# Optimization experiments

Hardware: AMD Instinct MI355X
Metric: run time of the kernel (lower is better)

Reference implementation:

```python
import jax, jax.numpy as jnp
import numpy as np

NUM_GROUPS = 32
EPS = 1e-5


def group_norm(x, gamma, beta):
    # x: [B, C, H, W]; normalize per group of C//NUM_GROUPS channels over (c_in_group, H, W)
    B, C, H, W = x.shape
    xg = x.reshape(B, NUM_GROUPS, C // NUM_GROUPS, H, W)
    mean = jnp.mean(xg, axis=(2, 3, 4), keepdims=True)
    var = jnp.var(xg, axis=(2, 3, 4), keepdims=True)
    xn = ((xg - mean) * jax.lax.rsqrt(var + EPS)).reshape(B, C, H, W)
    return xn * gamma[None, :, None, None] + beta[None, :, None, None]


def setup_inputs() -> dict:
    key = jax.random.key(0)
    kx, kq, kp = jax.random.split(key, 3)
    B, C, H, W = 4, 256, 64, 64
    x = jax.random.normal(kx, (B, C, H, W), dtype=jnp.float32)
    gamma = jnp.ones((C,), dtype=jnp.float32)
    beta = jnp.zeros((C,), dtype=jnp.float32)
    # 1x1 convs == channel matmuls; weights [out_c, in_c]
    w_qkv = jax.random.normal(kq, (3 * C, C), dtype=jnp.float32) / np.sqrt(C)
    w_proj = jax.random.normal(kp, (C, C), dtype=jnp.float32) / np.sqrt(C)
    return {"x": x, "t": 0, "gamma": gamma, "beta": beta, "w_qkv": w_qkv, "w_proj": w_proj}


def reference(x, t, gamma, beta, w_qkv, w_proj):
    B, C, H, W = x.shape
    normed = group_norm(x, gamma, beta)  # [B,C,H,W]
    qkv = jnp.einsum('bchw,oc->bohw', normed, w_qkv)  # [B,3C,H,W]
    q, k, v = jnp.split(qkv, 3, axis=1)
    N = H * W
    q = q.reshape(B, C, N)
    k = k.reshape(B, C, N)
    v = v.reshape(B, C, N)
    # scores[b,i,j] = sum_c q[b,c,i] k[b,c,j] / sqrt(C)
    scores = jnp.einsum('bci,bcj->bij', q, k) / jnp.sqrt(jnp.asarray(C, x.dtype))
    attn = jax.nn.softmax(scores, axis=-1)  # [B,N,N]
    # out[b,c,i] = sum_j v[b,c,j] attn[b,i,j]
    out = jnp.einsum('bcj,bij->bci', v, attn).reshape(B, C, H, W)
    out = jnp.einsum('bchw,oc->bohw', out, w_proj)
    return x + out
```

## Files before the change

### kernel.cpp

```cpp
#include <hip/hip_runtime.h>

typedef __bf16 bf16x8 __attribute__((ext_vector_type(8)));
typedef float floatx4 __attribute__((ext_vector_type(4)));
typedef float floatx16 __attribute__((ext_vector_type(16)));
typedef unsigned int u32;
typedef unsigned long long u64;

#define BB 4
#define CC 256
#define NN 4096

__device__ __forceinline__ unsigned short f2bf(float f) {
  union { float f; unsigned u; } v; v.f = f;
  unsigned r = v.u + 0x7fffu + ((v.u >> 16) & 1u);
  return (unsigned short)(r >> 16);
}

__device__ __forceinline__ float bf2f(unsigned short s) {
  union { unsigned u; float f; } v; v.u = ((u32)s) << 16;
  return v.f;
}

__device__ __forceinline__ void async16(const void* g, void* l) {
  __builtin_amdgcn_global_load_lds((const __attribute__((address_space(1))) u32*)g,
                                   (__attribute__((address_space(3))) u32*)l, 16, 0, 0);
}

__device__ __forceinline__ u32 fbits(float f) {
  union { float f; u32 u; } v; v.f = f; return v.u;
}

__global__ __launch_bounds__(256) void gn_fused(const float* __restrict__ x,
                                                const float* __restrict__ gamma, const float* __restrict__ beta,
                                                unsigned short* __restrict__ normed,
                                                const float* __restrict__ wqkv, const float* __restrict__ wproj,
                                                unsigned short* __restrict__ wq_bf, unsigned short* __restrict__ wp_bf) {
  int t = threadIdx.x;
  if (blockIdx.x >= 128) {
    int base = (blockIdx.x - 128) * 1024;
#pragma unroll
    for (int j = 0; j < 4; ++j) {
      int i = base + j * 256 + t;
      if (i < 196608) {
        float v = wqkv[i];
        if (i < 65536) v *= 0.090168440055560213f;
        wq_bf[i] = f2bf(v);
      } else {
        wp_bf[i - 196608] = f2bf(wproj[i - 196608]);
      }
    }
    return;
  }

  __shared__ __attribute__((aligned(16))) char smem[65928];
  unsigned short* xs = (unsigned short*)smem;
  float* par = (float*)(smem + 65664);

  int bg = blockIdx.x;
  int g = bg & 31;
  const float* p = x + (size_t)bg * 32768;
  float s = 0.f, q = 0.f;
#pragma unroll
  for (int it = 0; it < 32; ++it) {
    int idx = it * 1024 + t * 4;
    float4 v = *(const float4*)(p + idx);
    s += v.x + v.y + v.z + v.w;
    q += v.x * v.x + v.y * v.y + v.z * v.z + v.w * v.w;
    u64 pk = (u64)f2bf(v.x) | ((u64)f2bf(v.y) << 16) | ((u64)f2bf(v.z) << 32) | ((u64)f2bf(v.w) << 48);
    int row = idx >> 12, col = idx & 4095;
    *(u64*)&xs[row * 4104 + col] = pk;
  }
#pragma unroll
  for (int off = 1; off < 64; off <<= 1) {
    s += __shfl_xor(s, off, 64);
    q += __shfl_xor(q, off, 64);
  }
  int w = t >> 6;
  if ((t & 63) == 0) { par[32 + w] = s; par[40 + w] = q; }
  __syncthreads();
  if (t == 0) {
    float S = par[32] + par[33] + par[34] + par[35];
    float Q = par[40] + par[41] + par[42] + par[43];
    float mean = S * (1.f / 32768.f);
    float var = Q * (1.f / 32768.f) - mean * mean;
    par[16] = mean;
    par[17] = rsqrtf(var + 1e-5f);
  }
  __syncthreads();
  if (t < 8) {
    float mean = par[16], rstd = par[17];
    float sc = rstd * gamma[g * 8 + t];
    par[t] = sc;
    par[8 + t] = beta[g * 8 + t] - mean * sc;
  }
  __syncthreads();
  float scv[8], shv[8];
#pragma unroll
  for (int c = 0; c < 8; ++c) { scv[c] = par[c]; shv[c] = par[8 + c]; }
  unsigned short* ob = normed + (size_t)bg * 4096 * 8;
#pragma unroll
  for (int k = 0; k < 16; ++k) {
    int n = k * 256 + t;
    union { unsigned short us[8]; uint4 qv; } o;
#pragma unroll
    for (int c = 0; c < 8; ++c) {
      float xv = bf2f(xs[c * 4104 + n]);
      o.us[c] = f2bf(xv * scv[c] + shv[c]);
    }
    *(uint4*)(ob + (size_t)n * 8) = o.qv;
  }
}

__global__ __launch_bounds__(256, 2) void gemm_qkv_v(const unsigned short* __restrict__ normed,
                                                     const unsigned short* __restrict__ wq_bf,
                                                     const unsigned short* __restrict__ wv_bf,
                                                     unsigned short* __restrict__ qkbuf,
                                                     unsigned short* __restrict__ vbuf) {
  __shared__ __attribute__((aligned(16))) char smem[65536];
  int b = blockIdx.y;
  const unsigned short *Ab, *Bb;
  unsigned short* Cb;
  int ldc, m0, n0;
  bool aBlocked;
  if (blockIdx.x < 128) {
    int mt = blockIdx.x % 32, nt = blockIdx.x / 32;
    m0 = mt * 128; n0 = nt * 128;
    Ab = normed + (size_t)b * NN * 8 * 32;
    Bb = wq_bf + (size_t)n0 * 256;
    Cb = qkbuf + (size_t)b * NN * 512;
    ldc = 512;
    aBlocked = true;
  } else {
    int xx = blockIdx.x - 128;
    int mt = xx & 1, nt = xx >> 1;
    m0 = mt * 128; n0 = nt * 128;
    Ab = wv_bf + (size_t)m0 * 256;
    Bb = normed + (size_t)b * NN * 8 * 32;
    Cb = vbuf + (size_t)b * CC * NN;
    ldc = NN;
    aBlocked = false;
  }
  int t = threadIdx.x, w = t >> 6, l = t & 63;
  int l16 = l & 15, quad = l >> 4;
  int wr = w >> 1, wc = w & 1;

  auto stage = [&](int kb, int buf) {
    int rsub = l >> 3;
    int cj = (l & 7) ^ rsub;
    char* ab = smem + buf * 16384;
    char* bb = smem + 32768 + buf * 16384;
#pragma unroll
    for (int it = 0; it < 4; ++it) {
      int pp = w * 4 + it;
      int row = 8 * pp + rsub;
      size_t goLin = (size_t)row * 256 + kb * 64 + cj * 8;
      if (aBlocked) {
        size_t goA = ((size_t)(kb * 8 + cj) * 4096 + m0 + row) * 8;
        async16(Ab + goA, ab + pp * 1024);
        async16(Bb + goLin, bb + pp * 1024);
      } else {
        size_t goB = ((size_t)(kb * 8 + cj) * 4096 + n0 + row) * 8;
        async16(Ab + goLin, ab + pp * 1024);
        async16(Bb + goB, bb + pp * 1024);
      }
    }
  };

  floatx4 acc[4][4];
#pragma unroll
  for (int m = 0; m < 4; ++m)
#pragma unroll
    for (int n = 0; n < 4; ++n)
#pragma unroll
      for (int r = 0; r < 4; ++r) acc[m][n][r] = 0.f;

  stage(0, 0);

#pragma unroll 1
  for (int kb = 0; kb < 4; ++kb) {
    int cur = kb & 1;
    __syncthreads();
    if (kb < 3) stage(kb + 1, cur ^ 1);
    const unsigned short* As = (const unsigned short*)(smem + cur * 16384);
    const unsigned short* Bs = (const unsigned short*)(smem + 32768 + cur * 16384);
#pragma unroll
    for (int kk = 0; kk < 2; ++kk) {
      bf16x8 af[4], bfr[4];
      int sw = ((kk * 4 + quad) ^ (l16 & 7)) * 8;
#pragma unroll
      for (int m = 0; m < 4; ++m)
        af[m] = *(const bf16x8*)&As[(wr * 64 + m * 16 + l16) * 64 + sw];
#pragma unroll
      for (int n = 0; n < 4; ++n)
        bfr[n] = *(const bf16x8*)&Bs[(wc * 64 + n * 16 + l16) * 64 + sw];
#pragma unroll
      for (int m = 0; m < 4; ++m)
#pragma unroll
        for (int n = 0; n < 4; ++n)
          acc[m][n] = __builtin_amdgcn_mfma_f32_16x16x32_bf16(af[m], bfr[n], acc[m][n], 0, 0, 0);
    }
  }

#pragma unroll
  for (int m = 0; m < 4; ++m)
#pragma unroll
    for (int n = 0; n < 4; ++n)
#pragma unroll
      for (int r = 0; r < 4; ++r) {
        int row = m0 + wr * 64 + m * 16 + quad * 4 + r;
        int col = n0 + wc * 64 + n * 16 + l16;
        Cb[(size_t)row * ldc + col] = f2bf(acc[m][n][r]);
      }
}

__global__ __launch_bounds__(512, 2) void attn(const unsigned short* __restrict__ qk,
                                               const unsigned short* __restrict__ vbuf,
                                               unsigned short* __restrict__ opart0,
                                               unsigned short* __restrict__ opart1,
                                               float* __restrict__ lpart) {
  __shared__ __attribute__((aligned(16))) char smem[131072];

  int xcd = blockIdx.x & 7, slot = blockIdx.x >> 3;
  int b = xcd >> 1;
  int kh = xcd & 1;
  int i0 = slot * 128;
  int k0 = kh * 32;

  int t = threadIdx.x, w = t >> 6, l = t & 63;
  int l31 = l & 31, hi = l >> 5;
  int jh = w & 1;
  int iq = w >> 1;

  const size_t bqk = (size_t)b * NN * 512;
  const size_t bv = (size_t)b * CC * NN;

  auto stage = [&](int tile, int buf) {
    const unsigned short* kg = qk + bqk + (size_t)tile * 64 * 512 + 256;
    char* kb = smem + buf * 32768;
#pragma unroll
    for (int it = 0; it < 4; ++it) {
      int pp = w * 4 + it;
      int r = 2 * pp + (l >> 5);
      int c = (l & 31) ^ (r & 31);
      async16(kg + (size_t)r * 512 + c * 8, kb + pp * 1024);
    }
    const unsigned short* vg = vbuf + bv + (size_t)tile * 64;
    char* vb = smem + 65536 + buf * 32768;
    int cj = (l & 7) ^ ((l >> 3) & 7);
#pragma unroll
    for (int it = 0; it < 4; ++it) {
      int pp = w * 4 + it;
      int rc = 8 * pp + (l >> 3);
      async16(vg + (size_t)rc * NN + cj * 8, vb + pp * 1024);
    }
  };

  stage(k0, 0);

  bf16x8 qreg[16];
  {
    const unsigned short* qp = qk + bqk + (size_t)(i0 + iq * 32 + l31) * 512 + hi * 8;
#pragma unroll
    for (int ks = 0; ks < 16; ++ks)
      qreg[ks] = *(const bf16x8*)(qp + ks * 16);
  }

  floatx16 oacc[8];
#pragma unroll
  for (int cf = 0; cf < 8; ++cf)
#pragma unroll
    for (int r = 0; r < 16; ++r) oacc[cf][r] = 0.f;
  float lacc = 0.f;

  for (int kt = 0; kt < 32; ++kt) {
    int cur = kt & 1;
    __syncthreads();
    if (kt < 31) stage(k0 + kt + 1, cur ^ 1);

    const unsigned short* Kc = (const unsigned short*)(smem + cur * 32768);
    const unsigned short* Vc = (const unsigned short*)(smem + 65536 + cur * 32768);

    floatx16 st;
#pragma unroll
    for (int r = 0; r < 16; ++r) st[r] = 0.f;
#pragma unroll
    for (int ks = 0; ks < 16; ++ks) {
      bf16x8 kf = *(const bf16x8*)&Kc[(jh * 32 + l31) * 256 + (((ks << 1) | hi) ^ l31) * 8];
      st = __builtin_amdgcn_mfma_f32_32x32x16_bf16(kf, qreg[ks], st, 0, 0, 0);
    }

    u32 pr[8];
#pragma unroll
    for (int k2 = 0; k2 < 8; ++k2) {
      float p0 = __builtin_amdgcn_exp2f(st[2 * k2]);
      float p1 = __builtin_amdgcn_exp2f(st[2 * k2 + 1]);
      lacc += p0 + p1;
      pr[k2] = __builtin_amdgcn_perm(fbits(p1), fbits(p0), 0x07060302u);
    }

    union U { u32 u[4]; bf16x8 v; } a0, a1;
    {
      u32 sA = hi ? pr[0] : pr[2], sB = hi ? pr[1] : pr[3];
      u32 rA = (u32)__shfl_xor((int)sA, 32, 64);
      u32 rB = (u32)__shfl_xor((int)sB, 32, 64);
      a0.u[0] = hi ? rA : pr[0]; a0.u[1] = hi ? rB : pr[1];
      a0.u[2] = hi ? pr[2] : rA; a0.u[3] = hi ? pr[3] : rB;
      sA = hi ? pr[4] : pr[6]; sB = hi ? pr[5] : pr[7];
      rA = (u32)__shfl_xor((int)sA, 32, 64);
      rB = (u32)__shfl_xor((int)sB, 32, 64);
      a1.u[0] = hi ? rA : pr[4]; a1.u[1] = hi ? rB : pr[5];
      a1.u[2] = hi ? pr[6] : rA; a1.u[3] = hi ? pr[7] : rB;
    }

#pragma unroll
    for (int cf = 0; cf < 8; ++cf) {
      const unsigned short* vrow = Vc + (cf * 32 + l31) * 64;
      bf16x8 v0 = *(const bf16x8*)(vrow + (((jh * 4) | hi) ^ (l31 & 7)) * 8);
      oacc[cf] = __builtin_amdgcn_mfma_f32_32x32x16_bf16(a0.v, v0, oacc[cf], 0, 0, 0);
      bf16x8 v1 = *(const bf16x8*)(vrow + (((jh * 4 + 2) | hi) ^ (l31 & 7)) * 8);
      oacc[cf] = __builtin_amdgcn_mfma_f32_32x32x16_bf16(a1.v, v1, oacc[cf], 0, 0, 0);
    }
  }

  float l2 = lacc + __shfl_xor(lacc, 32, 64);

  float* Of = (float*)smem + iq * 8192;
  __syncthreads();
  if (jh == 1) {
#pragma unroll
    for (int cf = 0; cf < 8; ++cf)
#pragma unroll
      for (int r = 0; r < 16; ++r) {
        int il = (r & 3) + 8 * (r >> 2) + 4 * hi;
        Of[il * 256 + cf * 32 + l31] = oacc[cf][r];
      }
  }
  __syncthreads();
  unsigned short* ops = kh ? opart1 : opart0;
  size_t rowbase = (size_t)b * NN + i0 + iq * 32;
  if (jh == 0) {
#pragma unroll
    for (int cf = 0; cf < 8; ++cf)
#pragma unroll
      for (int r = 0; r < 16; ++r) {
        int il = (r & 3) + 8 * (r >> 2) + 4 * hi;
        float v = oacc[cf][r] + Of[il * 256 + cf * 32 + l31];
        ops[(rowbase + il) * CC + cf * 32 + l31] = f2bf(v);
      }
  }
  __syncthreads();
  float* Lred = (float*)smem;
  if (hi == 0) Lred[w * 32 + l31] = l2;
  __syncthreads();
  if (jh == 0 && hi == 0) {
    size_t pbl = (size_t)(b * 2 + kh) * NN + i0;
    lpart[pbl + iq * 32 + l31] = Lred[(iq * 2) * 32 + l31] + Lred[(iq * 2 + 1) * 32 + l31];
  }
}

__global__ __launch_bounds__(256, 2) void gemm_proj(const unsigned short* __restrict__ wp,
                                                    const unsigned short* __restrict__ op0,
                                                    const unsigned short* __restrict__ op1,
                                                    const float* __restrict__ lp,
                                                    float* __restrict__ out, const float* __restrict__ x) {
  __shared__ __attribute__((aligned(16))) char smem[51456];
  int mt = blockIdx.x & 1;
  int nt = blockIdx.x >> 1;
  int b = blockIdx.y;
  int m0 = mt * 128, n0 = nt * 64;
  int t = threadIdx.x, w = t >> 6, l = t & 63;
  int l16 = l & 15, quad = l >> 4;
  int wr = w >> 1, wc = w & 1;
  const unsigned short* Ab = wp + (size_t)m0 * 256;
  float* Linv = (float*)(smem + 51200);

  auto stageA = [&](int kb, int buf) {
    int rsub = l >> 3;
    int cj = (l & 7) ^ rsub;
    char* ab = smem + buf * 16384;
#pragma unroll
    for (int it = 0; it < 4; ++it) {
      int pp = w * 4 + it;
      size_t go = (size_t)(8 * pp + rsub) * 256 + kb * 64 + cj * 8;
      async16(Ab + go, ab + pp * 1024);
    }
  };

  int brow = t >> 2;
  int bck = (t & 3) * 16;
  size_t bgo_base = ((size_t)b * NN + n0 + brow) * 256 + bck;
  uint4 b0a, b0b, b1a, b1b;
  auto loadB = [&](int kb) {
    size_t go = bgo_base + kb * 64;
    b0a = *(const uint4*)(op0 + go);
    b0b = *(const uint4*)(op0 + go + 8);
    b1a = *(const uint4*)(op1 + go);
    b1b = *(const uint4*)(op1 + go + 8);
  };

  if (t < 64) Linv[t] = 1.f / (lp[b * 8192 + n0 + t] + lp[b * 8192 + 4096 + n0 + t]);
  stageA(0, 0);
  loadB(0);
  __syncthreads();

  floatx4 acc[4][2];
#pragma unroll
  for (int m = 0; m < 4; ++m)
#pragma unroll
    for (int n = 0; n < 2; ++n)
#pragma unroll
      for (int r = 0; r < 4; ++r) acc[m][n][r] = 0.f;

#pragma unroll 1
  for (int kb = 0; kb < 4; ++kb) {
    int cur = kb & 1;
    {
      float li = Linv[brow];
      unsigned short* Bs = (unsigned short*)(smem + 32768 + cur * 9216);
      const unsigned short* pa = (const unsigned short*)&b0a;
      const unsigned short* pc = (const unsigned short*)&b1a;
      union { unsigned short us[8]; uint4 q; } o1_, o2_;
#pragma unroll
      for (int j = 0; j < 8; ++j) o1_.us[j] = f2bf((bf2f(pa[j]) + bf2f(pc[j])) * li);
      pa = (const unsigned short*)&b0b;
      pc = (const unsigned short*)&b1b;
#pragma unroll
      for (int j = 0; j < 8; ++j) o2_.us[j] = f2bf((bf2f(pa[j]) + bf2f(pc[j])) * li);
      *(uint4*)&Bs[brow * 72 + bck] = o1_.q;
      *(uint4*)&Bs[brow * 72 + bck + 8] = o2_.q;
    }
    if (kb < 3) loadB(kb + 1);
    __syncthreads();
    if (kb < 3) stageA(kb + 1, cur ^ 1);
    const unsigned short* As = (const unsigned short*)(smem + cur * 16384);
    const unsigned short* Bs = (const unsigned short*)(smem + 32768 + cur * 9216);
#pragma unroll
    for (int kk = 0; kk < 2; ++kk) {
      bf16x8 af[4], bfr[2];
      int sw = ((kk * 4 + quad) ^ (l16 & 7)) * 8;
#pragma unroll
      for (int m = 0; m < 4; ++m)
        af[m] = *(const bf16x8*)&As[(wr * 64 + m * 16 + l16) * 64 + sw];
#pragma unroll
      for (int n = 0; n < 2; ++n)
        bfr[n] = *(const bf16x8*)&Bs[(wc * 32 + n * 16 + l16) * 72 + kk * 32 + quad * 8];
#pragma unroll
      for (int m = 0; m < 4; ++m)
#pragma unroll
        for (int n = 0; n < 2; ++n)
          acc[m][n] = __builtin_amdgcn_mfma_f32_16x16x32_bf16(af[m], bfr[n], acc[m][n], 0, 0, 0);
    }
  }

  size_t cb = (size_t)b * CC * NN;
#pragma unroll
  for (int m = 0; m < 4; ++m)
#pragma unroll
    for (int n = 0; n < 2; ++n)
#pragma unroll
      for (int r = 0; r < 4; ++r) {
        int row = m0 + wr * 64 + m * 16 + quad * 4 + r;
        int col = n0 + wc * 32 + n * 16 + l16;
        size_t idx = cb + (size_t)row * NN + col;
        out[idx] = acc[m][n][r] + x[idx];
      }
}

extern "C" void kernel_launch(void* const* d_in, const int* in_sizes, int n_in,
                              void* d_out, int out_size, void* d_ws, size_t ws_size,
                              hipStream_t stream) {
  const float* x     = (const float*)d_in[0];
  const float* gamma = (const float*)d_in[2];
  const float* beta  = (const float*)d_in[3];
  const float* wqkv  = (const float*)d_in[4];
  const float* wproj = (const float*)d_in[5];
  float* out = (float*)d_out;

  char* p = (char*)d_ws;
  unsigned short* wq_bf   = (unsigned short*)(p + 1024);
  unsigned short* wp_bf   = (unsigned short*)(p + 394240);
  unsigned short* normed  = (unsigned short*)(p + 525312);
  unsigned short* qkbuf   = (unsigned short*)(p + 8913920);
  unsigned short* vbuf    = (unsigned short*)(p + 25691136);
  unsigned short* opart1  = (unsigned short*)(p + 34079744);
  unsigned short* opart0  = normed;
  float* lpart            = (float*)(p + 1024);
  unsigned short* wv_bf   = wq_bf + 512 * 256;

  gn_fused<<<384, 256, 0, stream>>>(x, gamma, beta, normed, wqkv, wproj, wq_bf, wp_bf);
  gemm_qkv_v<<<dim3(192, 4), 256, 0, stream>>>(normed, wq_bf, wv_bf, qkbuf, vbuf);
  attn<<<256, 512, 0, stream>>>(qkbuf, vbuf, opart0, opart1, lpart);
  gemm_proj<<<dim3(128, 4), 256, 0, stream>>>(wp_bf, opart0, opart1, lpart, out, x);
}
```

Measured before the change: 186.6 us.

## Fuse all four stages into one cooperative persistent kernel with grid syncs

Replaces the four separate launches (groupnorm, QKV GEMM, attention, projection GEMM) with a single cooperative kernel of 256 blocks by 512 threads. Grid-wide syncs separate the stages. The GEMM stages run two 256-thread virtual blocks per real block over separate halves of shared memory. This removes kernel launch gaps and tail drain between stages. In exchange it adds grid-sync cost, caps the grid at 256 blocks with a large shared allocation, and makes the GEMM stages loop over more virtual tiles per block.

```diff
diff --git a/kernel.cpp b/kernel.cpp
--- a/kernel.cpp
+++ b/kernel.cpp
@@ -1,4 +1,7 @@
 #include <hip/hip_runtime.h>
+#include <hip/hip_cooperative_groups.h>
+
+namespace cg = cooperative_groups;
 
 typedef __bf16 bf16x8 __attribute__((ext_vector_type(8)));
 typedef float floatx4 __attribute__((ext_vector_type(4)));
@@ -30,440 +33,447 @@
   union { float f; u32 u; } v; v.f = f; return v.u;
 }
 
-__global__ __launch_bounds__(256) void gn_fused(const float* __restrict__ x,
-                                                const float* __restrict__ gamma, const float* __restrict__ beta,
-                                                unsigned short* __restrict__ normed,
-                                                const float* __restrict__ wqkv, const float* __restrict__ wproj,
-                                                unsigned short* __restrict__ wq_bf, unsigned short* __restrict__ wp_bf) {
-  int t = threadIdx.x;
-  if (blockIdx.x >= 128) {
-    int base = (blockIdx.x - 128) * 1024;
-#pragma unroll
-    for (int j = 0; j < 4; ++j) {
-      int i = base + j * 256 + t;
-      if (i < 196608) {
-        float v = wqkv[i];
-        if (i < 65536) v *= 0.090168440055560213f;
-        wq_bf[i] = f2bf(v);
+__global__ __launch_bounds__(512, 2) void mega(
+    const float* __restrict__ x, const float* __restrict__ gamma, const float* __restrict__ beta,
+    const float* __restrict__ wqkv, const float* __restrict__ wproj,
+    unsigned short* __restrict__ wq_bf, unsigned short* __restrict__ wp_bf,
+    unsigned short* __restrict__ normed,
+    unsigned short* __restrict__ qkbuf, unsigned short* __restrict__ vbuf,
+    unsigned short* __restrict__ opart1, float* __restrict__ lpart,
+    float* __restrict__ out) {
+  __shared__ __attribute__((aligned(16))) char smem[131072];
+  cg::grid_group grid = cg::this_grid();
+  const unsigned short* wv_bf = wq_bf + 512 * 256;
+
+  {
+    int tid = threadIdx.x;
+    if (blockIdx.x >= 128) {
+      int base = (blockIdx.x - 128) * 2048;
+#pragma unroll
+      for (int j = 0; j < 4; ++j) {
+        int i = base + j * 512 + tid;
+        if (i < 196608) {
+          float v = wqkv[i];
+          if (i < 65536) v *= 0.090168440055560213f;
+          wq_bf[i] = f2bf(v);
+        } else {
+          wp_bf[i - 196608] = f2bf(wproj[i - 196608]);
+        }
+      }
+    } else {
+      unsigned short* xs = (unsigned short*)smem;
+      float* par = (float*)(smem + 65664);
+      int bg = blockIdx.x;
+      int g = bg & 31;
+      const float* p = x + (size_t)bg * 32768;
+      float s = 0.f, q = 0.f;
+#pragma unroll
+      for (int it = 0; it < 16; ++it) {
+        int idx = it * 2048 + tid * 4;
+        float4 v = *(const float4*)(p + idx);
+        s += v.x + v.y + v.z + v.w;
+        q += v.x * v.x + v.y * v.y + v.z * v.z + v.w * v.w;
+        u64 pk = (u64)f2bf(v.x) | ((u64)f2bf(v.y) << 16) | ((u64)f2bf(v.z) << 32) | ((u64)f2bf(v.w) << 48);
+        int row = idx >> 12, col = idx & 4095;
+        *(u64*)&xs[row * 4104 + col] = pk;
+      }
+#pragma unroll
+      for (int off = 1; off < 64; off <<= 1) {
+        s += __shfl_xor(s, off, 64);
+        q += __shfl_xor(q, off, 64);
+      }
+      int w8 = tid >> 6;
+      if ((tid & 63) == 0) { par[32 + w8] = s; par[40 + w8] = q; }
+      __syncthreads();
+      if (tid == 0) {
+        float S = 0.f, Q = 0.f;
+#pragma unroll
+        for (int i = 0; i < 8; ++i) { S += par[32 + i]; Q += par[40 + i]; }
+        float mean = S * (1.f / 32768.f);
+        float var = Q * (1.f / 32768.f) - mean * mean;
+        par[16] = mean;
+        par[17] = rsqrtf(var + 1e-5f);
+      }
+      __syncthreads();
+      if (tid < 8) {
+        float mean = par[16], rstd = par[17];
+        float sc = rstd * gamma[g * 8 + tid];
+        par[tid] = sc;
+        par[8 + tid] = beta[g * 8 + tid] - mean * sc;
+      }
+      __syncthreads();
+      float scv[8], shv[8];
+#pragma unroll
+      for (int c = 0; c < 8; ++c) { scv[c] = par[c]; shv[c] = par[8 + c]; }
+      unsigned short* ob = normed + (size_t)bg * 32768;
+#pragma unroll
+      for (int k = 0; k < 8; ++k) {
+        int n = k * 512 + tid;
+        union { unsigned short us[8]; uint4 qv; } o;
+#pragma unroll
+        for (int c = 0; c < 8; ++c)
+          o.us[c] = f2bf(bf2f(xs[c * 4104 + n]) * scv[c] + shv[c]);
+        *(uint4*)(ob + (size_t)n * 8) = o.qv;
+      }
+    }
+  }
+
+  grid.sync();
+
+  {
+    int half = threadIdx.x >> 8;
+    int t = threadIdx.x & 255;
+    char* hs = smem + half * 65536;
+    int w = t >> 6, l = t & 63;
+    int l16 = l & 15, quad = l >> 4;
+    int wr = w >> 1, wc = w & 1;
+#pragma unroll 1
+    for (int it2 = 0; it2 < 2; ++it2) {
+      int vb = blockIdx.x * 2 + half + it2 * 512;
+      bool active = vb < 768;
+      int vx = active ? vb % 192 : 0;
+      int b = active ? vb / 192 : 0;
+      const unsigned short *Ab, *Bb;
+      unsigned short* Cb;
+      int ldc, m0, n0;
+      bool aBlocked;
+      if (vx < 128) {
+        int mt = vx % 32, nt = vx / 32;
+        m0 = mt * 128; n0 = nt * 128;
+        Ab = normed + (size_t)b * NN * 8 * 32;
+        Bb = wq_bf + (size_t)n0 * 256;
+        Cb = qkbuf + (size_t)b * NN * 512;
+        ldc = 512;
+        aBlocked = true;
       } else {
-        wp_bf[i - 196608] = f2bf(wproj[i - 196608]);
-      }
-    }
-    return;
+        int xx = vx - 128;
+        int mt = xx & 1, nt = xx >> 1;
+        m0 = mt * 128; n0 = nt * 128;
+        Ab = wv_bf + (size_t)m0 * 256;
+        Bb = normed + (size_t)b * NN * 8 * 32;
+        Cb = vbuf + (size_t)b * CC * NN;
+        ldc = NN;
+        aBlocked = false;
+      }
+      auto stage = [&](int kb, int buf) {
+        int rsub = l >> 3;
+        int cj = (l & 7) ^ rsub;
+        char* ab = hs + buf * 16384;
+        char* bb = hs + 32768 + buf * 16384;
+#pragma unroll
+        for (int it = 0; it < 4; ++it) {
+          int pp = w * 4 + it;
+          int row = 8 * pp + rsub;
+          size_t goLin = (size_t)row * 256 + kb * 64 + cj * 8;
+          if (aBlocked) {
+            size_t goA = ((size_t)(kb * 8 + cj) * 4096 + m0 + row) * 8;
+            async16(Ab + goA, ab + pp * 1024);
+            async16(Bb + goLin, bb + pp * 1024);
+          } else {
+            size_t goB = ((size_t)(kb * 8 + cj) * 4096 + n0 + row) * 8;
+            async16(Ab + goLin, ab + pp * 1024);
+            async16(Bb + goB, bb + pp * 1024);
+          }
+        }
+      };
+      floatx4 acc[4][4];
+#pragma unroll
+      for (int m = 0; m < 4; ++m)
+#pragma unroll
+        for (int n = 0; n < 4; ++n)
+#pragma unroll
+          for (int r = 0; r < 4; ++r) acc[m][n][r] = 0.f;
+      if (active) stage(0, 0);
+#pragma unroll 1
+      for (int kb = 0; kb < 4; ++kb) {
+        int cur = kb & 1;
+        __syncthreads();
+        if (active) {
+          if (kb < 3) stage(kb + 1, cur ^ 1);
+          const unsigned short* As = (const unsigned short*)(hs + cur * 16384);
+          const unsigned short* Bs = (const unsigned short*)(hs + 32768 + cur * 16384);
+#pragma unroll
+          for (int kk = 0; kk < 2; ++kk) {
+            bf16x8 af[4], bfr[4];
+            int sw = ((kk * 4 + quad) ^ (l16 & 7)) * 8;
+#pragma unroll
+            for (int m = 0; m < 4; ++m)
+              af[m] = *(const bf16x8*)&As[(wr * 64 + m * 16 + l16) * 64 + sw];
+#pragma unroll
+            for (int n = 0; n < 4; ++n)
+              bfr[n] = *(const bf16x8*)&Bs[(wc * 64 + n * 16 + l16) * 64 + sw];
+#pragma unroll
+            for (int m = 0; m < 4; ++m)
+#pragma unroll
+              for (int n = 0; n < 4; ++n)
+                acc[m][n] = __builtin_amdgcn_mfma_f32_16x16x32_bf16(af[m], bfr[n], acc[m][n], 0, 0, 0);
+          }
+        }
+      }
+      if (active) {
+#pragma unroll
+        for (int m = 0; m < 4; ++m)
+#pragma unroll
+          for (int n = 0; n < 4; ++n)
+#pragma unroll
+            for (int r = 0; r < 4; ++r) {
+              int row = m0 + wr * 64 + m * 16 + quad * 4 + r;
+              int col = n0 + wc * 64 + n * 16 + l16;
+              Cb[(size_t)row * ldc + col] = f2bf(acc[m][n][r]);
+            }
+      }
+    }
   }
 
-  __shared__ __attribute__((aligned(16))) char smem[65928];
-  unsigned short* xs = (unsigned short*)smem;
-  float* par = (float*)(smem + 65664);
-
-  int bg = blockIdx.x;
-  int g = bg & 31;
-  const float* p = x + (size_t)bg * 32768;
-  float s = 0.f, q = 0.f;
-#pragma unroll
-  for (int it = 0; it < 32; ++it) {
-    int idx = it * 1024 + t * 4;
-    float4 v = *(const float4*)(p + idx);
-    s += v.x + v.y + v.z + v.w;
-    q += v.x * v.x + v.y * v.y + v.z * v.z + v.w * v.w;
-    u64 pk = (u64)f2bf(v.x) | ((u64)f2bf(v.y) << 16) | ((u64)f2bf(v.z) << 32) | ((u64)f2bf(v.w) << 48);
-    int row = idx >> 12, col = idx & 4095;
-    *(u64*)&xs[row * 4104 + col] = pk;
+  grid.sync();
+
+  {
+    int xcd = blockIdx.x & 7, slot = blockIdx.x >> 3;
+    int b = xcd >> 1;
+    int kh = xcd & 1;
+    int i0 = slot * 128;
+    int k0 = kh * 32;
+
+    int t = threadIdx.x, w = t >> 6, l = t & 63;
+    int l31 = l & 31, hi = l >> 5;
+    int jh = w & 1;
+    int iq = w >> 1;
+
+    const size_t bqk = (size_t)b * NN * 512;
+    const size_t bv = (size_t)b * CC * NN;
+
+    auto stage = [&](int tile, int buf) {
+      const unsigned short* kg = qkbuf + bqk + (size_t)tile * 64 * 512 + 256;
+      char* kb = smem + buf * 32768;
+#pragma unroll
+      for (int it = 0; it < 4; ++it) {
+        int pp = w * 4 + it;
+        int r = 2 * pp + (l >> 5);
+        int c = (l & 31) ^ (r & 31);
+        async16(kg + (size_t)r * 512 + c * 8, kb + pp * 1024);
+      }
+      const unsigned short* vg = vbuf + bv + (size_t)tile * 64;
+      char* vb2 = smem + 65536 + buf * 32768;
+      int cj = (l & 7) ^ ((l >> 3) & 7);
+#pragma unroll
+      for (int it = 0; it < 4; ++it) {
+        int pp = w * 4 + it;
+        int rc = 8 * pp + (l >> 3);
+        async16(vg + (size_t)rc * NN + cj * 8, vb2 + pp * 1024);
+      }
+    };
+
+    stage(k0, 0);
+
+    bf16x8 qreg[16];
+    {
+      const unsigned short* qp = qkbuf + bqk + (size_t)(i0 + iq * 32 + l31) * 512 + hi * 8;
+#pragma unroll
+      for (int ks = 0; ks < 16; ++ks)
+        qreg[ks] = *(const bf16x8*)(qp + ks * 16);
+    }
+
+    floatx16 oacc[8];
+#pragma unroll
+    for (int cf = 0; cf < 8; ++cf)
+#pragma unroll
+      for (int r = 0; r < 16; ++r) oacc[cf][r] = 0.f;
+    float lacc = 0.f;
+
+    for (int kt = 0; kt < 32; ++kt) {
+      int cur = kt & 1;
+      __syncthreads();
+      if (kt < 31) stage(k0 + kt + 1, cur ^ 1);
+
+      const unsigned short* Kc = (const unsigned short*)(smem + cur * 32768);
+      const unsigned short* Vc = (const unsigned short*)(smem + 65536 + cur * 32768);
+
+      floatx16 st;
+#pragma unroll
+      for (int r = 0; r < 16; ++r) st[r] = 0.f;
+#pragma unroll
+      for (int ks = 0; ks < 16; ++ks) {
+        bf16x8 kf = *(const bf16x8*)&Kc[(jh * 32 + l31) * 256 + (((ks << 1) | hi) ^ l31) * 8];
+        st = __builtin_amdgcn_mfma_f32_32x32x16_bf16(kf, qreg[ks], st, 0, 0, 0);
+      }
+
+      u32 pr[8];
+#pragma unroll
+      for (int k2 = 0; k2 < 8; ++k2) {
+        float p0 = __builtin_amdgcn_exp2f(st[2 * k2]);
+        float p1 = __builtin_amdgcn_exp2f(st[2 * k2 + 1]);
+        lacc += p0 + p1;
+        pr[k2] = __builtin_amdgcn_perm(fbits(p1), fbits(p0), 0x07060302u);
+      }
+
+      union U { u32 u[4]; bf16x8 v; } a0, a1;
+      {
+        u32 sA = hi ? pr[0] : pr[2], sB = hi ? pr[1] : pr[3];
+        u32 rA = (u32)__shfl_xor((int)sA, 32, 64);
+        u32 rB = (u32)__shfl_xor((int)sB, 32, 64);
+        a0.u[0] = hi ? rA : pr[0]; a0.u[1] = hi ? rB : pr[1];
+        a0.u[2] = hi ? pr[2] : rA; a0.u[3] = hi ? pr[3] : rB;
+        sA = hi ? pr[4] : pr[6]; sB = hi ? pr[5] : pr[7];
+        rA = (u32)__shfl_xor((int)sA, 32, 64);
+        rB = (u32)__shfl_xor((int)sB, 32, 64);
+        a1.u[0] = hi ? rA : pr[4]; a1.u[1] = hi ? rB : pr[5];
+        a1.u[2] = hi ? pr[6] : rA; a1.u[3] = hi ? pr[7] : rB;
+      }
+
+#pragma unroll
+      for (int cf = 0; cf < 8; ++cf) {
+        const unsigned short* vrow = Vc + (cf * 32 + l31) * 64;
+        bf16x8 v0 = *(const bf16x8*)(vrow + (((jh * 4) | hi) ^ (l31 & 7)) * 8);
+        oacc[cf] = __builtin_amdgcn_mfma_f32_32x32x16_bf16(a0.v, v0, oacc[cf], 0, 0, 0);
+        bf16x8 v1 = *(const bf16x8*)(vrow + (((jh * 4 + 2) | hi) ^ (l31 & 7)) * 8);
+        oacc[cf] = __builtin_amdgcn_mfma_f32_32x32x16_bf16(a1.v, v1, oacc[cf], 0, 0, 0);
+      }
+    }
+
+    float l2 = lacc + __shfl_xor(lacc, 32, 64);
+
+    float* Of = (float*)smem + iq * 8192;
+    __syncthreads();
+    if (jh == 1) {
+#pragma unroll
+      for (int cf = 0; cf < 8; ++cf)
+#pragma unroll
+        for (int r = 0; r < 16; ++r) {
+          int il = (r & 3) + 8 * (r >> 2) + 4 * hi;
+          Of[il * 256 + cf * 32 + l31] = oacc[cf][r];
+        }
+    }
+    __syncthreads();
+    unsigned short* ops = kh ? opart1 : normed;
+    size_t rowbase = (size_t)b * NN + i0 + iq * 32;
+    if (jh == 0) {
+#pragma unroll
+      for (int cf = 0; cf < 8; ++cf)
+#pragma unroll
+        for (int r = 0; r < 16; ++r) {
+          int il = (r & 3) + 8 * (r >> 2) + 4 * hi;
+          float v = oacc[cf][r] + Of[il * 256 + cf * 32 + l31];
+          ops[(rowbase + il) * CC + cf * 32 + l31] = f2bf(v);
+        }
+    }
+    __syncthreads();
+    float* Lred = (float*)smem;
+    if (hi == 0) Lred[w * 32 + l31] = l2;
+    __syncthreads();
+    if (jh == 0 && hi == 0) {
+      size_t pbl = (size_t)(b * 2 + kh) * NN + i0;
+      lpart[pbl + iq * 32 + l31] = Lred[(iq * 2) * 32 + l31] + Lred[(iq * 2 + 1) * 32 + l31];
+    }
   }
-#pragma unroll
-  for (int off = 1; off < 64; off <<= 1) {
-    s += __shfl_xor(s, off, 64);
-    q += __shfl_xor(q, off, 64);
+
+  grid.sync();
+
+  {
+    int half = threadIdx.x >> 8;
+    int t = threadIdx.x & 255;
+    char* hs = smem + half * 65536;
+    int vb = blockIdx.x * 2 + half;
+    int vx = vb & 127, b = vb >> 7;
+    int mt = vx & 1, nt = vx >> 1;
+    int m0 = mt * 128, n0 = nt * 64;
+    int w = t >> 6, l = t & 63;
+    int l16 = l & 15, quad = l >> 4;
+    int wr = w >> 1, wc = w & 1;
+    const unsigned short* Ab = wp_bf + (size_t)m0 * 256;
+    const unsigned short* op0 = normed;
+    float* Linv = (float*)(hs + 51200);
+
+    auto stageA = [&](int kb, int buf) {
+      int rsub = l >> 3;
+      int cj = (l & 7) ^ rsub;
+      char* ab = hs + buf * 16384;
+#pragma unroll
+      for (int it = 0; it < 4; ++it) {
+        int pp = w * 4 + it;
+        size_t go = (size_t)(8 * pp + rsub) * 256 + kb * 64 + cj * 8;
+        async16(Ab + go, ab + pp * 1024);
+      }
+    };
+
+    int brow = t >> 2;
+    int bck = (t & 3) * 16;
+    size_t bgo_base = ((size_t)b * NN + n0 + brow) * 256 + bck;
+    uint4 b0a, b0b, b1a, b1b;
+    auto loadB = [&](int kb) {
+      size_t go = bgo_base + kb * 64;
+      b0a = *(const uint4*)(op0 + go);
+      b0b = *(const uint4*)(op0 + go + 8);
+      b1a = *(const uint4*)(opart1 + go);
+      b1b = *(const uint4*)(opart1 + go + 8);
+    };
+
+    if (t < 64) Linv[t] = 1.f / (lpart[b * 8192 + n0 + t] + lpart[b * 8192 + 4096 + n0 + t]);
+    stageA(0, 0);
+    loadB(0);
+    __syncthreads();
+
+    floatx4 acc[4][2];
+#pragma unroll
+    for (int m = 0; m < 4; ++m)
+#pragma unroll
+      for (int n = 0; n < 2; ++n)
+#pragma unroll
+        for (int r = 0; r < 4; ++r) acc[m][n][r] = 0.f;
+
+#pragma unroll 1
+    for (int kb = 0; kb < 4; ++kb) {
+      int cur = kb & 1;
+      {
+        float li = Linv[brow];
+        unsigned short* Bs = (unsigned short*)(hs + 32768 + cur * 9216);
+        const unsigned short* pa = (const unsigned short*)&b0a;
+        const unsigned short* pc = (const unsigned short*)&b1a;
+        union { unsigned short us[8]; uint4 q; } o1_, o2_;
+#pragma unroll
+        for (int j = 0; j < 8; ++j) o1_.us[j] = f2bf((bf2f(pa[j]) + bf2f(pc[j])) * li);
+        pa = (const unsigned short*)&b0b;
+        pc = (const unsigned short*)&b1b;
+#pragma unroll
+        for (int j = 0; j < 8; ++j) o2_.us[j] = f2bf((bf2f(pa[j]) + bf2f(pc[j])) * li);
+        *(uint4*)&Bs[brow * 72 + bck] = o1_.q;
+        *(uint4*)&Bs[brow * 72 + bck + 8] = o2_.q;
+      }
+      if (kb < 3) loadB(kb + 1);
+      __syncthreads();
+      if (kb < 3) stageA(kb + 1, cur ^ 1);
+      const unsigned short* As = (const unsigned short*)(hs + cur * 16384);
+      const unsigned short* Bs = (const unsigned short*)(hs + 32768 + cur * 9216);
+#pragma unroll
+      for (int kk = 0; kk < 2; ++kk) {
+        bf16x8 af[4], bfr[2];
+        int sw = ((kk * 4 + quad) ^ (l16 & 7)) * 8;
+#pragma unroll
+        for (int m = 0; m < 4; ++m)
+          af[m] = *(const bf16x8*)&As[(wr * 64 + m * 16 + l16) * 64 + sw];
+#pragma unroll
+        for (int n = 0; n < 2; ++n)
+          bfr[n] = *(const bf16x8*)&Bs[(wc * 32 + n * 16 + l16) * 72 + kk * 32 + quad * 8];
+#pragma unroll
+        for (int m = 0; m < 4; ++m)
+#pragma unroll
+          for (int n = 0; n < 2; ++n)
+            acc[m][n] = __builtin_amdgcn_mfma_f32_16x16x32_bf16(af[m], bfr[n], acc[m][n], 0, 0, 0);
+      }
+    }
+
+    size_t cb = (size_t)b * CC * NN;
+#pragma unroll
+    for (int m = 0; m < 4; ++m)
+#pragma unroll
+      for (int n = 0; n < 2; ++n)
+#pragma unroll
+        for (int r = 0; r < 4; ++r) {
+          int row = m0 + wr * 64 + m * 16 + quad * 4 + r;
+          int col = n0 + wc * 32 + n * 16 + l16;
+          size_t idx = cb + (size_t)row * NN + col;
+          out[idx] = acc[m][n][r] + x[idx];
+        }
   }
-  int w = t >> 6;
-  if ((t & 63) == 0) { par[32 + w] = s; par[40 + w] = q; }
-  __syncthreads();
-  if (t == 0) {
-    float S = par[32] + par[33] + par[34] + par[35];
-    float Q = par[40] + par[41] + par[42] + par[43];
-    float mean = S * (1.f / 32768.f);
-    float var = Q * (1.f / 32768.f) - mean * mean;
-    par[16] = mean;
-    par[17] = rsqrtf(var + 1e-5f);
-  }
-  __syncthreads();
-  if (t < 8) {
-    float mean = par[16], rstd = par[17];
-    float sc = rstd * gamma[g * 8 + t];
-    par[t] = sc;
-    par[8 + t] = beta[g * 8 + t] - mean * sc;
-  }
-  __syncthreads();
-  float scv[8], shv[8];
-#pragma unroll
-  for (int c = 0; c < 8; ++c) { scv[c] = par[c]; shv[c] = par[8 + c]; }
-  unsigned short* ob = normed + (size_t)bg * 4096 * 8;
-#pragma unroll
-  for (int k = 0; k < 16; ++k) {
-    int n = k * 256 + t;
-    union { unsigned short us[8]; uint4 qv; } o;
-#pragma unroll
-    for (int c = 0; c < 8; ++c) {
-      float xv = bf2f(xs[c * 4104 + n]);
-      o.us[c] = f2bf(xv * scv[c] + shv[c]);
-    }
-    *(uint4*)(ob + (size_t)n * 8) = o.qv;
-  }
-}
-
-__global__ __launch_bounds__(256, 2) void gemm_qkv_v(const unsigned short* __restrict__ normed,
-                                                     const unsigned short* __restrict__ wq_bf,
-                                                     const unsigned short* __restrict__ wv_bf,
-                                                     unsigned short* __restrict__ qkbuf,
-                                                     unsigned short* __restrict__ vbuf) {
-  __shared__ __attribute__((aligned(16))) char smem[65536];
-  int b = blockIdx.y;
-  const unsigned short *Ab, *Bb;
-  unsigned short* Cb;
-  int ldc, m0, n0;
-  bool aBlocked;
-  if (blockIdx.x < 128) {
-    int mt = blockIdx.x % 32, nt = blockIdx.x / 32;
-    m0 = mt * 128; n0 = nt * 128;
-    Ab = normed + (size_t)b * NN * 8 * 32;
-    Bb = wq_bf + (size_t)n0 * 256;
-    Cb = qkbuf + (size_t)b * NN * 512;
-    ldc = 512;
-    aBlocked = true;
-  } else {
-    int xx = blockIdx.x - 128;
-    int mt = xx & 1, nt = xx >> 1;
-    m0 = mt * 128; n0 = nt * 128;
-    Ab = wv_bf + (size_t)m0 * 256;
-    Bb = normed + (size_t)b * NN * 8 * 32;
-    Cb = vbuf + (size_t)b * CC * NN;
-    ldc = NN;
-    aBlocked = false;
-  }
-  int t = threadIdx.x, w = t >> 6, l = t & 63;
-  int l16 = l & 15, quad = l >> 4;
-  int wr = w >> 1, wc = w & 1;
-
-  auto stage = [&](int kb, int buf) {
-    int rsub = l >> 3;
-    int cj = (l & 7) ^ rsub;
-    char* ab = smem + buf * 16384;
-    char* bb = smem + 32768 + buf * 16384;
-#pragma unroll
-    for (int it = 0; it < 4; ++it) {
-      int pp = w * 4 + it;
-      int row = 8 * pp + rsub;
-      size_t goLin = (size_t)row * 256 + kb * 64 + cj * 8;
-      if (aBlocked) {
-        size_t goA = ((size_t)(kb * 8 + cj) * 4096 + m0 + row) * 8;
-        async16(Ab + goA, ab + pp * 1024);
-        async16(Bb + goLin, bb + pp * 1024);
-      } else {
-        size_t goB = ((size_t)(kb * 8 + cj) * 4096 + n0 + row) * 8;
-        async16(Ab + goLin, ab + pp * 1024);
-        async16(Bb + goB, bb + pp * 1024);
-      }
-    }
-  };
-
-  floatx4 acc[4][4];
-#pragma unroll
-  for (int m = 0; m < 4; ++m)
-#pragma unroll
-    for (int n = 0; n < 4; ++n)
-#pragma unroll
-      for (int r = 0; r < 4; ++r) acc[m][n][r] = 0.f;
-
-  stage(0, 0);
-
-#pragma unroll 1
-  for (int kb = 0; kb < 4; ++kb) {
-    int cur = kb & 1;
-    __syncthreads();
-    if (kb < 3) stage(kb + 1, cur ^ 1);
-    const unsigned short* As = (const unsigned short*)(smem + cur * 16384);
-    const unsigned short* Bs = (const unsigned short*)(smem + 32768 + cur * 16384);
-#pragma unroll
-    for (int kk = 0; kk < 2; ++kk) {
-      bf16x8 af[4], bfr[4];
-      int sw = ((kk * 4 + quad) ^ (l16 & 7)) * 8;
-#pragma unroll
-      for (int m = 0; m < 4; ++m)
-        af[m] = *(const bf16x8*)&As[(wr * 64 + m * 16 + l16) * 64 + sw];
-#pragma unroll
-      for (int n = 0; n < 4; ++n)
-        bfr[n] = *(const bf16x8*)&Bs[(wc * 64 + n * 16 + l16) * 64 + sw];
-#pragma unroll
-      for (int m = 0; m < 4; ++m)
-#pragma unroll
-        for (int n = 0; n < 4; ++n)
-          acc[m][n] = __builtin_amdgcn_mfma_f32_16x16x32_bf16(af[m], bfr[n], acc[m][n], 0, 0, 0);
-    }
-  }
-
-#pragma unroll
-  for (int m = 0; m < 4; ++m)
-#pragma unroll
-    for (int n = 0; n < 4; ++n)
-#pragma unroll
-      for (int r = 0; r < 4; ++r) {
-        int row = m0 + wr * 64 + m * 16 + quad * 4 + r;
-        int col = n0 + wc * 64 + n * 16 + l16;
-        Cb[(size_t)row * ldc + col] = f2bf(acc[m][n][r]);
-      }
-}
-
-__global__ __launch_bounds__(512, 2) void attn(const unsigned short* __restrict__ qk,
-                                               const unsigned short* __restrict__ vbuf,
-                                               unsigned short* __restrict__ opart0,
-                                               unsigned short* __restrict__ opart1,
-                                               float* __restrict__ lpart) {
-  __shared__ __attribute__((aligned(16))) char smem[131072];
-
-  int xcd = blockIdx.x & 7, slot = blockIdx.x >> 3;
-  int b = xcd >> 1;
-  int kh = xcd & 1;
-  int i0 = slot * 128;
-  int k0 = kh * 32;
-
-  int t = threadIdx.x, w = t >> 6, l = t & 63;
-  int l31 = l & 31, hi = l >> 5;
-  int jh = w & 1;
-  int iq = w >> 1;
-
-  const size_t bqk = (size_t)b * NN * 512;
-  const size_t bv = (size_t)b * CC * NN;
-
-  auto stage = [&](int tile, int buf) {
-    const unsigned short* kg = qk + bqk + (size_t)tile * 64 * 512 + 256;
-    char* kb = smem + buf * 32768;
-#pragma unroll
-    for (int it = 0; it < 4; ++it) {
-      int pp = w * 4 + it;
-      int r = 2 * pp + (l >> 5);
-      int c = (l & 31) ^ (r & 31);
-      async16(kg + (size_t)r * 512 + c * 8, kb + pp * 1024);
-    }
-    const unsigned short* vg = vbuf + bv + (size_t)tile * 64;
-    char* vb = smem + 65536 + buf * 32768;
-    int cj = (l & 7) ^ ((l >> 3) & 7);
-#pragma unroll
-    for (int it = 0; it < 4; ++it) {
-      int pp = w * 4 + it;
-      int rc = 8 * pp + (l >> 3);
-      async16(vg + (size_t)rc * NN + cj * 8, vb + pp * 1024);
-    }
-  };
-
-  stage(k0, 0);
-
-  bf16x8 qreg[16];
-  {
-    const unsigned short* qp = qk + bqk + (size_t)(i0 + iq * 32 + l31) * 512 + hi * 8;
-#pragma unroll
-    for (int ks = 0; ks < 16; ++ks)
-      qreg[ks] = *(const bf16x8*)(qp + ks * 16);
-  }
-
-  floatx16 oacc[8];
-#pragma unroll
-  for (int cf = 0; cf < 8; ++cf)
-#pragma unroll
-    for (int r = 0; r < 16; ++r) oacc[cf][r] = 0.f;
-  float lacc = 0.f;
-
-  for (int kt = 0; kt < 32; ++kt) {
-    int cur = kt & 1;
-    __syncthreads();
-    if (kt < 31) stage(k0 + kt + 1, cur ^ 1);
-
-    const unsigned short* Kc = (const unsigned short*)(smem + cur * 32768);
-    const unsigned short* Vc = (const unsigned short*)(smem + 65536 + cur * 32768);
-
-    floatx16 st;
-#pragma unroll
-    for (int r = 0; r < 16; ++r) st[r] = 0.f;
-#pragma unroll
-    for (int ks = 0; ks < 16; ++ks) {
-      bf16x8 kf = *(const bf16x8*)&Kc[(jh * 32 + l31) * 256 + (((ks << 1) | hi) ^ l31) * 8];
-      st = __builtin_amdgcn_mfma_f32_32x32x16_bf16(kf, qreg[ks], st, 0, 0, 0);
-    }
-
-    u32 pr[8];
-#pragma unroll
-    for (int k2 = 0; k2 < 8; ++k2) {
-      float p0 = __builtin_amdgcn_exp2f(st[2 * k2]);
-      float p1 = __builtin_amdgcn_exp2f(st[2 * k2 + 1]);
-      lacc += p0 + p1;
-      pr[k2] = __builtin_amdgcn_perm(fbits(p1), fbits(p0), 0x07060302u);
-    }
-
-    union U { u32 u[4]; bf16x8 v; } a0, a1;
-    {
-      u32 sA = hi ? pr[0] : pr[2], sB = hi ? pr[1] : pr[3];
-      u32 rA = (u32)__shfl_xor((int)sA, 32, 64);
-      u32 rB = (u32)__shfl_xor((int)sB, 32, 64);
-      a0.u[0] = hi ? rA : pr[0]; a0.u[1] = hi ? rB : pr[1];
-      a0.u[2] = hi ? pr[2] : rA; a0.u[3] = hi ? pr[3] : rB;
-      sA = hi ? pr[4] : pr[6]; sB = hi ? pr[5] : pr[7];
-      rA = (u32)__shfl_xor((int)sA, 32, 64);
-      rB = (u32)__shfl_xor((int)sB, 32, 64);
-      a1.u[0] = hi ? rA : pr[4]; a1.u[1] = hi ? rB : pr[5];
-      a1.u[2] = hi ? pr[6] : rA; a1.u[3] = hi ? pr[7] : rB;
-    }
-
-#pragma unroll
-    for (int cf = 0; cf < 8; ++cf) {
-      const unsigned short* vrow = Vc + (cf * 32 + l31) * 64;
-      bf16x8 v0 = *(const bf16x8*)(vrow + (((jh * 4) | hi) ^ (l31 & 7)) * 8);
-      oacc[cf] = __builtin_amdgcn_mfma_f32_32x32x16_bf16(a0.v, v0, oacc[cf], 0, 0, 0);
-      bf16x8 v1 = *(const bf16x8*)(vrow + (((jh * 4 + 2) | hi) ^ (l31 & 7)) * 8);
-      oacc[cf] = __builtin_amdgcn_mfma_f32_32x32x16_bf16(a1.v, v1, oacc[cf], 0, 0, 0);
-    }
-  }
-
-  float l2 = lacc + __shfl_xor(lacc, 32, 64);
-
-  float* Of = (float*)smem + iq * 8192;
-  __syncthreads();
-  if (jh == 1) {
-#pragma unroll
-    for (int cf = 0; cf < 8; ++cf)
-#pragma unroll
-      for (int r = 0; r < 16; ++r) {
-        int il = (r & 3) + 8 * (r >> 2) + 4 * hi;
-        Of[il * 256 + cf * 32 + l31] = oacc[cf][r];
-      }
-  }
-  __syncthreads();
-  unsigned short* ops = kh ? opart1 : opart0;
-  size_t rowbase = (size_t)b * NN + i0 + iq * 32;
-  if (jh == 0) {
-#pragma unroll
-    for (int cf = 0; cf < 8; ++cf)
-#pragma unroll
-      for (int r = 0; r < 16; ++r) {
-        int il = (r & 3) + 8 * (r >> 2) + 4 * hi;
-        float v = oacc[cf][r] + Of[il * 256 + cf * 32 + l31];
-        ops[(rowbase + il) * CC + cf * 32 + l31] = f2bf(v);
-      }
-  }
-  __syncthreads();
-  float* Lred = (float*)smem;
-  if (hi == 0) Lred[w * 32 + l31] = l2;
-  __syncthreads();
-  if (jh == 0 && hi == 0) {
-    size_t pbl = (size_t)(b * 2 + kh) * NN + i0;
-    lpart[pbl + iq * 32 + l31] = Lred[(iq * 2) * 32 + l31] + Lred[(iq * 2 + 1) * 32 + l31];
-  }
-}
-
-__global__ __launch_bounds__(256, 2) void gemm_proj(const unsigned short* __restrict__ wp,
-                                                    const unsigned short* __restrict__ op0,
-                                                    const unsigned short* __restrict__ op1,
-                                                    const float* __restrict__ lp,
-                                                    float* __restrict__ out, const float* __restrict__ x) {
-  __shared__ __attribute__((aligned(16))) char smem[51456];
-  int mt = blockIdx.x & 1;
-  int nt = blockIdx.x >> 1;
-  int b = blockIdx.y;
-  int m0 = mt * 128, n0 = nt * 64;
-  int t = threadIdx.x, w = t >> 6, l = t & 63;
-  int l16 = l & 15, quad = l >> 4;
-  int wr = w >> 1, wc = w & 1;
-  const unsigned short* Ab = wp + (size_t)m0 * 256;
-  float* Linv = (float*)(smem + 51200);
-
-  auto stageA = [&](int kb, int buf) {
-    int rsub = l >> 3;
-    int cj = (l & 7) ^ rsub;
-    char* ab = smem + buf * 16384;
-#pragma unroll
-    for (int it = 0; it < 4; ++it) {
-      int pp = w * 4 + it;
-      size_t go = (size_t)(8 * pp + rsub) * 256 + kb * 64 + cj * 8;
-      async16(Ab + go, ab + pp * 1024);
-    }
-  };
-
-  int brow = t >> 2;
-  int bck = (t & 3) * 16;
-  size_t bgo_base = ((size_t)b * NN + n0 + brow) * 256 + bck;
-  uint4 b0a, b0b, b1a, b1b;
-  auto loadB = [&](int kb) {
-    size_t go = bgo_base + kb * 64;
-    b0a = *(const uint4*)(op0 + go);
-    b0b = *(const uint4*)(op0 + go + 8);
-    b1a = *(const uint4*)(op1 + go);
-    b1b = *(const uint4*)(op1 + go + 8);
-  };
-
-  if (t < 64) Linv[t] = 1.f / (lp[b * 8192 + n0 + t] + lp[b * 8192 + 4096 + n0 + t]);
-  stageA(0, 0);
-  loadB(0);
-  __syncthreads();
-
-  floatx4 acc[4][2];
-#pragma unroll
-  for (int m = 0; m < 4; ++m)
-#pragma unroll
-    for (int n = 0; n < 2; ++n)
-#pragma unroll
-      for (int r = 0; r < 4; ++r) acc[m][n][r] = 0.f;
-
-#pragma unroll 1
-  for (int kb = 0; kb < 4; ++kb) {
-    int cur = kb & 1;
-    {
-      float li = Linv[brow];
-      unsigned short* Bs = (unsigned short*)(smem + 32768 + cur * 9216);
-      const unsigned short* pa = (const unsigned short*)&b0a;
-      const unsigned short* pc = (const unsigned short*)&b1a;
-      union { unsigned short us[8]; uint4 q; } o1_, o2_;
-#pragma unroll
-      for (int j = 0; j < 8; ++j) o1_.us[j] = f2bf((bf2f(pa[j]) + bf2f(pc[j])) * li);
-      pa = (const unsigned short*)&b0b;
-      pc = (const unsigned short*)&b1b;
-#pragma unroll
-      for (int j = 0; j < 8; ++j) o2_.us[j] = f2bf((bf2f(pa[j]) + bf2f(pc[j])) * li);
-      *(uint4*)&Bs[brow * 72 + bck] = o1_.q;
-      *(uint4*)&Bs[brow * 72 + bck + 8] = o2_.q;
-    }
-    if (kb < 3) loadB(kb + 1);
-    __syncthreads();
-    if (kb < 3) stageA(kb + 1, cur ^ 1);
-    const unsigned short* As = (const unsigned short*)(smem + cur * 16384);
-    const unsigned short* Bs = (const unsigned short*)(smem + 32768 + cur * 9216);
-#pragma unroll
-    for (int kk = 0; kk < 2; ++kk) {
-      bf16x8 af[4], bfr[2];
-      int sw = ((kk * 4 + quad) ^ (l16 & 7)) * 8;
-#pragma unroll
-      for (int m = 0; m < 4; ++m)
-        af[m] = *(const bf16x8*)&As[(wr * 64 + m * 16 + l16) * 64 + sw];
-#pragma unroll
-      for (int n = 0; n < 2; ++n)
-        bfr[n] = *(const bf16x8*)&Bs[(wc * 32 + n * 16 + l16) * 72 + kk * 32 + quad * 8];
-#pragma unroll
-      for (int m = 0; m < 4; ++m)
-#pragma unroll
-        for (int n = 0; n < 2; ++n)
-          acc[m][n] = __builtin_amdgcn_mfma_f32_16x16x32_bf16(af[m], bfr[n], acc[m][n], 0, 0, 0);
-    }
-  }
-
-  size_t cb = (size_t)b * CC * NN;
-#pragma unroll
-  for (int m = 0; m < 4; ++m)
-#pragma unroll
-    for (int n = 0; n < 2; ++n)
-#pragma unroll
-      for (int r = 0; r < 4; ++r) {
-        int row = m0 + wr * 64 + m * 16 + quad * 4 + r;
-        int col = n0 + wc * 32 + n * 16 + l16;
-        size_t idx = cb + (size_t)row * NN + col;
-        out[idx] = acc[m][n][r] + x[idx];
-      }
 }
 
 extern "C" void kernel_launch(void* const* d_in, const int* in_sizes, int n_in,
@@ -483,12 +493,10 @@
   unsigned short* qkbuf   = (unsigned short*)(p + 8913920);
   unsigned short* vbuf    = (unsigned short*)(p + 25691136);
   unsigned short* opart1  = (unsigned short*)(p + 34079744);
-  unsigned short* opart0  = normed;
   float* lpart            = (float*)(p + 1024);
-  unsigned short* wv_bf   = wq_bf + 512 * 256;
-
-  gn_fused<<<384, 256, 0, stream>>>(x, gamma, beta, normed, wqkv, wproj, wq_bf, wp_bf);
-  gemm_qkv_v<<<dim3(192, 4), 256, 0, stream>>>(normed, wq_bf, wv_bf, qkbuf, vbuf);
-  attn<<<256, 512, 0, stream>>>(qkbuf, vbuf, opart0, opart1, lpart);
-  gemm_proj<<<dim3(128, 4), 256, 0, stream>>>(wp_bf, opart0, opart1, lpart, out, x);
+
+  void* args[] = {(void*)&x, (void*)&gamma, (void*)&beta, (void*)&wqkv, (void*)&wproj,
+                  (void*)&wq_bf, (void*)&wp_bf, (void*)&normed, (void*)&qkbuf, (void*)&vbuf,
+                  (void*)&opart1, (void*)&lpart, (void*)&out};
+  hipLaunchCooperativeKernel((const void*)mega, dim3(256), dim3(512), args, 0, stream);
 }
```

New measurement: 302.1 us. 61.9% more time.
